# Kernel optimization log

Hardware: AMD Instinct MI355X
Metric: run time of the kernel (lower is better)

The kernel has to match this reference:

```python
import jax, jax.numpy as jnp
import numpy as np

B, M, H, K, D, L = 4, 1024, 1024, 16, 64, 1024
E, DH, TOPK = 8, 4096, 2
EPS = 1e-5


def _skew(X, pad_value):
    # X: [BK, M, L] -> [BK, M, M+L], row i shifted i steps right
    bk, m, l = X.shape
    X = jnp.pad(X, ((0, 0), (0, 0), (0, m + 1)), constant_values=pad_value)
    X = X.reshape(bk, -1)[:, :-m]
    return X.reshape(bk, m, m + l)


def _unskew(X):
    # X: [BK, M, M+L] -> [BK, M, L]
    bk, m, lp = X.shape
    l = lp - m
    X = X.reshape(bk, -1)
    X = jnp.pad(X, ((0, 0), (0, m)))
    X = X.reshape(bk, m, m + l + 1)
    return X[:, :, :l]


def layernorm(x, g, b):
    mu = jnp.mean(x, axis=-1, keepdims=True)
    var = jnp.var(x, axis=-1, keepdims=True)
    return (x - mu) * jax.lax.rsqrt(var + EPS) * g + b


def setup_inputs() -> dict:
    key = jax.random.key(0)
    ks = jax.random.split(key, 16)
    s = 1.0 / np.sqrt(H)
    inp = {
        'h': jax.random.normal(ks[0], (B, M, H), jnp.float32),
        'h_cache': jax.random.normal(ks[1], (B, L, H), jnp.float32),
        'key_pe': jax.random.normal(ks[2], (1, D, L), jnp.float32) * s,
        'wq': jax.random.normal(ks[3], (H, H), jnp.float32) * s,
        'wk': jax.random.normal(ks[4], (H, H), jnp.float32) * s,
        'wv': jax.random.normal(ks[5], (H, H), jnp.float32) * s,
        'wo': jax.random.normal(ks[6], (H, H), jnp.float32) * s,
        'norm1_g': jnp.ones((H,), jnp.float32),
        'norm1_b': jnp.zeros((H,), jnp.float32),
        'norm2_g': jnp.ones((H,), jnp.float32),
        'norm2_b': jnp.zeros((H,), jnp.float32),
        'moe_ln_g': jnp.ones((H,), jnp.float32),
        'moe_ln_b': jnp.zeros((H,), jnp.float32),
        'gate_w': jax.random.normal(ks[7], (H, E), jnp.float32) * s,
        'gate_b': jnp.zeros((E,), jnp.float32),
        'e_w1': jax.random.normal(ks[8], (E, H, DH), jnp.float32) * s,
        'e_b1': jnp.zeros((E, DH), jnp.float32),
        'e_w2': jax.random.normal(ks[9], (E, DH, H), jnp.float32) * (1.0 / np.sqrt(DH)),
        'e_b2': jnp.zeros((E, H), jnp.float32),
    }
    return inp


def _forward(h, h_cache, key_pe, wq, wk, wv, wo, norm1_g, norm1_b, norm2_g, norm2_b,
             moe_ln_g, moe_ln_b, gate_w, gate_b, e_w1, e_b1, e_w2, e_b2):
    h_all = jnp.concatenate([h_cache, h], axis=1)  # [B, L+M, H]

    def heads(x):  # [B, T, H] -> [B*K, T, D]
        b, t, _ = x.shape
        return x.reshape(b, t, K, D).transpose(0, 2, 1, 3).reshape(b * K, t, D)

    q = heads(h @ wq)          # [BK, M, D]
    k = heads(h_all @ wk)      # [BK, L+M, D]
    v = heads(h_all @ wv)      # [BK, L+M, D]

    attn_cont = jnp.einsum('bmd,bnd->bmn', q, k)      # [BK, M, L+M]
    attn_cont = _unskew(attn_cont)                     # [BK, M, L]
    attn_pos = jnp.einsum('bmd,dl->bml', q, key_pe[0])  # [BK, M, L]
    attn = (attn_cont + attn_pos) / np.sqrt(D)
    attn = jax.nn.softmax(attn, axis=-1)
    attn_sk = _skew(attn, 0.0)                         # [BK, M, M+L]
    out = jnp.einsum('bmn,bnd->bmd', attn_sk, v)       # [BK, M, D]
    out = out.reshape(B, K, M, D).transpose(0, 2, 1, 3).reshape(B, M, H)
    attn_out = out @ wo
    h = layernorm(h + attn_out, norm1_g, norm1_b)

    # --- MoE FFN (naive top-k gate, post-LN inside, dropout=0) ---
    x = h.reshape(-1, H)                               # [T, H]
    logits = x @ gate_w + gate_b                       # [T, E]
    vals, idx = jax.lax.top_k(logits, TOPK)            # [T, k]
    scores = jax.nn.softmax(vals, axis=-1)             # [T, k]
    hid = jax.nn.relu(jnp.einsum('th,ehd->etd', x, e_w1) + e_b1[:, None, :])
    all_out = jnp.einsum('etd,edh->eth', hid, e_w2) + e_b2[:, None, :]  # [E, T, H]
    sel = jnp.take_along_axis(all_out.transpose(1, 0, 2), idx[:, :, None], axis=1)  # [T, k, H]
    moe = jnp.sum(scores[:, :, None] * sel, axis=1)    # [T, H]
    core = layernorm(x + moe, moe_ln_g, moe_ln_b).reshape(B, M, H)
    h = layernorm(h + core, norm2_g, norm2_b)
    return h


def reference(h, h_cache, key_pe, wq, wk, wv, wo, norm1_g, norm1_b, norm2_g, norm2_b,
              moe_ln_g, moe_ln_b, gate_w, gate_b, e_w1, e_b1, e_w2, e_b2):
    return _forward(h, h_cache, key_pe, wq, wk, wv, wo, norm1_g, norm1_b, norm2_g,
                    norm2_b, moe_ln_g, moe_ln_b, gate_w, gate_b, e_w1, e_b1, e_w2, e_b2)
```

## Files before the change

### kernel.cpp

```cpp
#include <hip/hip_runtime.h>

typedef unsigned short u16;
typedef unsigned int u32;
typedef __attribute__((ext_vector_type(8))) __bf16 bf16x8;
typedef __attribute__((ext_vector_type(8))) _Float16 f16x8;
typedef __attribute__((ext_vector_type(4))) float f32x4;

__device__ __forceinline__ u16 f2bf(float f){
  unsigned int u = __float_as_uint(f);
  u += 0x7FFFu + ((u >> 16) & 1u);
  return (u16)(u >> 16);
}
__device__ __forceinline__ float bf2f(u16 s){
  return __uint_as_float(((unsigned int)s) << 16);
}
__device__ __forceinline__ void fsplit(float x, u16& hi, u16& lo){
  _Float16 h = (_Float16)x;
  float r = x - (float)h;
  _Float16 l = (_Float16)r;
  hi = *(u16*)&h; lo = *(u16*)&l;
}
__device__ __forceinline__ void gll16(const u16* g, u16* lds){
  __builtin_amdgcn_global_load_lds(
      (const __attribute__((address_space(1))) u32*)g,
      (__attribute__((address_space(3))) u32*)(u32)(unsigned long long)lds,
      16, 0, 0);
}


__global__ void zero8(int* c){ if (threadIdx.x < 8) c[threadIdx.x] = 0; }

__global__ __launch_bounds__(256)
void transpose_cvt_z(const float* __restrict__ in, u16* __restrict__ outp,
                     int R, int C, long zin, long zout)
{
  __shared__ float tile[32][33];
  in  += (long)blockIdx.z * zin;
  outp+= (long)blockIdx.z * zout;
  const int c0 = blockIdx.x << 5, r0 = blockIdx.y << 5;
  const int tx = threadIdx.x, ty = threadIdx.y;
  #pragma unroll
  for (int i = ty; i < 32; i += 8)
    tile[i][tx] = in[(long)(r0 + i) * C + c0 + tx];
  __syncthreads();
  #pragma unroll
  for (int i = ty; i < 32; i += 8)
    outp[(long)(c0 + i) * R + r0 + tx] = f2bf(tile[tx][i]);
}

__global__ __launch_bounds__(256)
void transpose_split4(const float* __restrict__ s0, const float* __restrict__ s1,
                      const float* __restrict__ s2, const float* __restrict__ s3,
                      u16* __restrict__ wall_h, u16* __restrict__ wall_l,
                      u16* __restrict__ wo_h, u16* __restrict__ wo_l)
{
  __shared__ float tile[32][33];
  const int z = blockIdx.z;
  const float* in = (z==0)?s0:(z==1)?s1:(z==2)?s2:s3;
  u16* oh = (z<3) ? (wall_h + (long)z*1024*1024) : wo_h;
  u16* ol = (z<3) ? (wall_l + (long)z*1024*1024) : wo_l;
  const int c0 = blockIdx.x << 5, r0 = blockIdx.y << 5;
  const int tx = threadIdx.x, ty = threadIdx.y;
  #pragma unroll
  for (int i = ty; i < 32; i += 8)
    tile[i][tx] = in[(long)(r0 + i) * 1024 + c0 + tx];
  __syncthreads();
  #pragma unroll
  for (int i = ty; i < 32; i += 8){
    u16 hh, ll;
    fsplit(tile[tx][i], hh, ll);
    oh[(long)(c0 + i) * 1024 + r0 + tx] = hh;
    ol[(long)(c0 + i) * 1024 + r0 + tx] = ll;
  }
}

__global__ __launch_bounds__(256)
void cvt_split_hall(const float* __restrict__ hc, const float* __restrict__ h,
                    u16* __restrict__ hi, u16* __restrict__ lo)
{
  long i4 = (long)blockIdx.x * 256 + threadIdx.x;
  long row = i4 >> 8;
  int c4 = (int)(i4 & 255);
  int b = (int)(row >> 11), tt = (int)(row & 2047);
  const float4* src = (const float4*)((tt < 1024) ? (hc + ((long)b*1024 + tt)*1024)
                                                  : (h  + ((long)b*1024 + (tt-1024))*1024));
  float4 v = src[c4];
  ushort4 h4, l4;
  fsplit(v.x, h4.x, l4.x); fsplit(v.y, h4.y, l4.y);
  fsplit(v.z, h4.z, l4.z); fsplit(v.w, h4.w, l4.w);
  ((ushort4*)hi)[i4] = h4;
  ((ushort4*)lo)[i4] = l4;
}

__global__ __launch_bounds__(128)
void pack_pe(const float* __restrict__ pe, u16* __restrict__ PEh, u16* __restrict__ PEl)
{
  const int jt = blockIdx.x;
  const int t = threadIdx.x;
  const int ks = t >> 6, lane = t & 63;
  const int fq = lane >> 4, fr = lane & 15;
  const long o = ((long)(jt*2 + ks)*64 + lane)*8;
  #pragma unroll
  for (int e = 0; e < 8; ++e){
    float v = pe[(long)(ks*32 + fq*8 + e)*1024 + jt*16 + fr];
    u16 hh, ll; fsplit(v, hh, ll);
    PEh[o+e] = hh; PEl[o+e] = ll;
  }
}


template<int EPI>
__global__ __launch_bounds__(256)
void gemm_sp(const u16* __restrict__ Ah_, const u16* __restrict__ Al_,
             const u16* __restrict__ Bh_, const u16* __restrict__ Bl_,
             float* __restrict__ C,
             u16* __restrict__ Kh, u16* __restrict__ Kl,
             u16* __restrict__ Vh, u16* __restrict__ Vl,
             u16* __restrict__ Qh, u16* __restrict__ Ql,
             int N, int Kd)
{
  __shared__ __align__(16) u16 Ahs[4096];
  __shared__ __align__(16) u16 Als[4096];
  __shared__ __align__(16) u16 Bhs[4096];
  __shared__ __align__(16) u16 Bls[4096];
  const int tm = blockIdx.y, tn = blockIdx.x;
  const int t = threadIdx.x;
  const int lane = t & 63, wv = t >> 6;
  const int wm = wv >> 1, wn = wv & 1;
  const int fr = lane & 15, fq = lane >> 4;

  const int r0l = 32*wv + (lane >> 2);
  const int r1l = r0l + 16;
  const int colu = (lane & 3) << 3;
  const long ar0 = (long)(tm*128 + r0l), ar1 = (long)(tm*128 + r1l);
  const long br0 = (long)(tn*128 + r0l), br1 = (long)(tn*128 + r1l);
  const u16* pah0 = Ah_ + ar0*Kd + colu;  const u16* pah1 = Ah_ + ar1*Kd + colu;
  const u16* pal0 = Al_ + ar0*Kd + colu;  const u16* pal1 = Al_ + ar1*Kd + colu;
  const u16* pbh0 = Bh_ + br0*Kd + colu;  const u16* pbh1 = Bh_ + br1*Kd + colu;
  const u16* pbl0 = Bl_ + br0*Kd + colu;  const u16* pbl1 = Bl_ + br1*Kd + colu;
  u16* lAh0 = Ahs + 1024*wv;  u16* lAh1 = lAh0 + 512;
  u16* lAl0 = Als + 1024*wv;  u16* lAl1 = lAl0 + 512;
  u16* lBh0 = Bhs + 1024*wv;  u16* lBh1 = lBh0 + 512;
  u16* lBl0 = Bls + 1024*wv;  u16* lBl1 = lBl0 + 512;

  f32x4 acc[4][4];
  const f32x4 z4 = {0.f,0.f,0.f,0.f};
  #pragma unroll
  for (int m=0;m<4;m++)
    #pragma unroll
    for (int n=0;n<4;n++) acc[m][n] = z4;

  const int nk = Kd >> 5;
  for (int kt = 0; kt < nk; ++kt) {
    const int ko = kt << 5;
    __syncthreads();
    gll16(pah0 + ko, lAh0); gll16(pah1 + ko, lAh1);
    gll16(pal0 + ko, lAl0); gll16(pal1 + ko, lAl1);
    gll16(pbh0 + ko, lBh0); gll16(pbh1 + ko, lBh1);
    gll16(pbl0 + ko, lBl0); gll16(pbl1 + ko, lBl1);
    __syncthreads();
    f16x8 afh[4], afl[4], bfh[4], bfl[4];
    #pragma unroll
    for (int m=0;m<4;m++){
      afh[m] = *(const f16x8*)(Ahs + (wm*64 + m*16 + fr)*32 + fq*8);
      afl[m] = *(const f16x8*)(Als + (wm*64 + m*16 + fr)*32 + fq*8);
    }
    #pragma unroll
    for (int n=0;n<4;n++){
      bfh[n] = *(const f16x8*)(Bhs + (wn*64 + n*16 + fr)*32 + fq*8);
      bfl[n] = *(const f16x8*)(Bls + (wn*64 + n*16 + fr)*32 + fq*8);
    }
    #pragma unroll
    for (int m=0;m<4;m++)
      #pragma unroll
      for (int n=0;n<4;n++){
        acc[m][n] = __builtin_amdgcn_mfma_f32_16x16x32_f16(afl[m], bfh[n], acc[m][n], 0, 0, 0);
        acc[m][n] = __builtin_amdgcn_mfma_f32_16x16x32_f16(afh[m], bfl[n], acc[m][n], 0, 0, 0);
        acc[m][n] = __builtin_amdgcn_mfma_f32_16x16x32_f16(afh[m], bfh[n], acc[m][n], 0, 0, 0);
      }
  }

  #pragma unroll
  for (int m=0;m<4;m++){
    #pragma unroll
    for (int j=0;j<4;j++){
      const long crow = (long)(tm*128 + wm*64 + m*16 + fq*4 + j);
      #pragma unroll
      for (int n=0;n<4;n++){
        const int c = tn*128 + wn*64 + n*16 + fr;
        float vv = acc[m][n][j];
        if (EPI == 0){
          C[crow * N + c] = vv;
        } else {
          const int b2 = (int)(crow >> 11), key = (int)(crow & 2047);
          u16 hh, ll; fsplit(vv, hh, ll);
          if (c < 1024){
            const int hd2 = c >> 6, dd = c & 63;
            const long addr = ((long)(b2*16 + hd2))*131072
                            + ((long)((key>>4)*2 + (dd>>5)))*512
                            + (((dd>>3)&3)*16 + (key&15))*8 + (dd&7);
            Kh[addr] = hh; Kl[addr] = ll;
          } else if (c < 2048){
            const int c2 = c - 1024;
            const int hd2 = c2 >> 6, dd = c2 & 63;
            const long addr = ((long)(b2*16 + hd2))*131072
                            + ((((long)(key>>4)*4 + (dd>>4))*2 + ((key>>3)&1)))*128
                            + (dd&15)*8 + (key&7);
            Vh[addr] = hh; Vl[addr] = ll;
          } else if (key >= 1024){
            const int c2 = c - 2048;
            const long qrow = (long)b2*1024 + (key - 1024);
            Qh[qrow*1024 + c2] = hh;
            Ql[qrow*1024 + c2] = ll;
          }
        }
      }
    }
  }
}


#define SJP 1032

__global__ __launch_bounds__(256)
void attn_mfma(const u16* __restrict__ qh, const u16* __restrict__ ql,
               const u16* __restrict__ Kph, const u16* __restrict__ Kpl,
               const u16* __restrict__ Vph, const u16* __restrict__ Vpl,
               const u16* __restrict__ PEh, const u16* __restrict__ PEl,
               u16* __restrict__ oh, u16* __restrict__ ol)
{
  __shared__ __align__(16) char smem[68608];
  float* Sj = (float*)smem;
  u16*   Ph = (u16*)smem;
  u16*   Pl = (u16*)(smem + 34048);
  const int bx = blockIdx.x;
  const int q0 = bx << 4;
  const int hd = blockIdx.y, b = blockIdx.z;
  const int t = threadIdx.x, lane = t & 63, wid = t >> 6;
  const int fr = lane & 15, fq = lane >> 4;
  const long plane = ((long)(b*16 + hd)) * 131072;

  f16x8 qfh[2], qfl[2];
  {
    const long qoff = ((long)(b*1024 + q0 + fr))*1024 + hd*64 + fq*8;
    qfh[0] = *(const f16x8*)(qh + qoff);
    qfh[1] = *(const f16x8*)(qh + qoff + 32);
    qfl[0] = *(const f16x8*)(ql + qoff);
    qfl[1] = *(const f16x8*)(ql + qoff + 32);
  }

  for (int base = 0; base < 65; base += 8){
    const int ta = base + wid;
    const int tb = base + wid + 4;
    const int tac = (ta < 65) ? ta : 64;
    const int tbc = (tb < 65) ? tb : 64;
    const u16* fA = Kph + plane + ((long)(bx + tac))*1024 + lane*8;
    const u16* fAl= Kpl + plane + ((long)(bx + tac))*1024 + lane*8;
    const u16* fB = Kph + plane + ((long)(bx + tbc))*1024 + lane*8;
    const u16* fBl= Kpl + plane + ((long)(bx + tbc))*1024 + lane*8;
    f32x4 accA = {0.f,0.f,0.f,0.f}, accB = {0.f,0.f,0.f,0.f};
    #pragma unroll
    for (int ks = 0; ks < 2; ++ks){
      f16x8 bhA = *(const f16x8*)(fA  + ks*512);
      f16x8 blA = *(const f16x8*)(fAl + ks*512);
      f16x8 bhB = *(const f16x8*)(fB  + ks*512);
      f16x8 blB = *(const f16x8*)(fBl + ks*512);
      accA = __builtin_amdgcn_mfma_f32_16x16x32_f16(qfl[ks], bhA, accA, 0, 0, 0);
      accB = __builtin_amdgcn_mfma_f32_16x16x32_f16(qfl[ks], bhB, accB, 0, 0, 0);
      accA = __builtin_amdgcn_mfma_f32_16x16x32_f16(qfh[ks], blA, accA, 0, 0, 0);
      accB = __builtin_amdgcn_mfma_f32_16x16x32_f16(qfh[ks], blB, accB, 0, 0, 0);
      accA = __builtin_amdgcn_mfma_f32_16x16x32_f16(qfh[ks], bhA, accA, 0, 0, 0);
      accB = __builtin_amdgcn_mfma_f32_16x16x32_f16(qfh[ks], bhB, accB, 0, 0, 0);
    }
    if (ta < 65){
      const int ca = tac*16 + fr;
      #pragma unroll
      for (int jj = 0; jj < 4; ++jj){
        const int row = fq*4 + jj;
        const int j = ca - row;
        if (j >= 0 && j < 1024) Sj[row*SJP + j] = accA[jj];
      }
    }
    if (tb < 65){
      const int cb = tbc*16 + fr;
      #pragma unroll
      for (int jj = 0; jj < 4; ++jj){
        const int row = fq*4 + jj;
        const int j = cb - row;
        if (j >= 0 && j < 1024) Sj[row*SJP + j] = accB[jj];
      }
    }
  }
  __syncthreads();

  for (int base = 0; base < 64; base += 8){
    const int ta = base + wid, tb = base + wid + 4;
    const u16* fA = PEh + ((long)ta)*1024 + lane*8;
    const u16* fAl= PEl + ((long)ta)*1024 + lane*8;
    const u16* fB = PEh + ((long)tb)*1024 + lane*8;
    const u16* fBl= PEl + ((long)tb)*1024 + lane*8;
    f32x4 accA = {0.f,0.f,0.f,0.f}, accB = {0.f,0.f,0.f,0.f};
    #pragma unroll
    for (int ks = 0; ks < 2; ++ks){
      f16x8 bhA = *(const f16x8*)(fA  + ks*512);
      f16x8 blA = *(const f16x8*)(fAl + ks*512);
      f16x8 bhB = *(const f16x8*)(fB  + ks*512);
      f16x8 blB = *(const f16x8*)(fBl + ks*512);
      accA = __builtin_amdgcn_mfma_f32_16x16x32_f16(qfl[ks], bhA, accA, 0, 0, 0);
      accB = __builtin_amdgcn_mfma_f32_16x16x32_f16(qfl[ks], bhB, accB, 0, 0, 0);
      accA = __builtin_amdgcn_mfma_f32_16x16x32_f16(qfh[ks], blA, accA, 0, 0, 0);
      accB = __builtin_amdgcn_mfma_f32_16x16x32_f16(qfh[ks], blB, accB, 0, 0, 0);
      accA = __builtin_amdgcn_mfma_f32_16x16x32_f16(qfh[ks], bhA, accA, 0, 0, 0);
      accB = __builtin_amdgcn_mfma_f32_16x16x32_f16(qfh[ks], bhB, accB, 0, 0, 0);
    }
    const int ja = ta*16 + fr, jb = tb*16 + fr;
    #pragma unroll
    for (int jj = 0; jj < 4; ++jj){
      const int row = fq*4 + jj;
      Sj[row*SJP + ja] += accA[jj];
      Sj[row*SJP + jb] += accB[jj];
    }
  }
  __syncthreads();

  {
    const int r = t >> 4, g = t & 15;
    float sv[64];
    float mx = -3.0e38f;
    #pragma unroll
    for (int m = 0; m < 64; ++m){
      float x = Sj[r*SJP + g + (m<<4)] * 0.125f;
      sv[m] = x; mx = fmaxf(mx, x);
    }
    #pragma unroll
    for (int o = 8; o; o >>= 1) mx = fmaxf(mx, __shfl_xor(mx, o, 64));
    float sum = 0.f;
    #pragma unroll
    for (int m = 0; m < 64; ++m){ sv[m] = __expf(sv[m] - mx); sum += sv[m]; }
    #pragma unroll
    for (int o = 8; o; o >>= 1) sum += __shfl_xor(sum, o, 64);
    const float inv = 1.f / sum;
    __syncthreads();
    for (int i = t; i < 17024; i += 256) ((unsigned*)smem)[i] = 0;
    __syncthreads();
    #pragma unroll
    for (int m = 0; m < 64; ++m){
      float p = sv[m] * inv;
      u16 hh, ll; fsplit(p, hh, ll);
      const int c = r + g + (m<<4);
      Ph[r*1064 + c] = hh;
      Pl[r*1064 + c] = ll;
    }
  }
  __syncthreads();

  {
    f32x4 acc0 = {0.f,0.f,0.f,0.f}, acc1 = {0.f,0.f,0.f,0.f};
    const int qq = fq & 1;
    for (int ks = 0; ks < 33; ++ks){
      int kc16 = bx + 2*ks + (fq >> 1);
      if (kc16 > 127) kc16 = 127;
      const long vo = plane + (((long)kc16*4 + wid)*2 + qq)*128 + fr*8;
      f16x8 vh = *(const f16x8*)(Vph + vo);
      f16x8 vl = *(const f16x8*)(Vpl + vo);
      f16x8 ah = *(const f16x8*)(Ph + fr*1064 + ks*32 + fq*8);
      f16x8 al = *(const f16x8*)(Pl + fr*1064 + ks*32 + fq*8);
      f32x4& a = (ks & 1) ? acc1 : acc0;
      a = __builtin_amdgcn_mfma_f32_16x16x32_f16(al, vh, a, 0, 0, 0);
      a = __builtin_amdgcn_mfma_f32_16x16x32_f16(ah, vl, a, 0, 0, 0);
      a = __builtin_amdgcn_mfma_f32_16x16x32_f16(ah, vh, a, 0, 0, 0);
    }
    #pragma unroll
    for (int jj = 0; jj < 4; ++jj){
      float v = acc0[jj] + acc1[jj];
      u16 hh, ll; fsplit(v, hh, ll);
      const int row = fq*4 + jj;
      const long o = ((long)(b*1024 + q0 + row))*1024 + hd*64 + wid*16 + fr;
      oh[o] = hh; ol[o] = ll;
    }
  }
}


template<bool GATHER, bool RELU>
__global__ __launch_bounds__(256)
void gemm_bt(const u16* __restrict__ A, const u16* __restrict__ Bt, u16* __restrict__ Cp,
             const float* __restrict__ bias, int N, int Kd, int maxA,
             const int* __restrict__ offs, const int* __restrict__ counts,
             const int* __restrict__ gather, int ebase)
{
  __shared__ __align__(16) u16 As[2][4096];
  __shared__ __align__(16) u16 Bs[2][4096];
  const int z = blockIdx.z;
  const int e = ebase + z;
  const int rbase = offs[e];
  const int cnt   = counts[e];
  const int tm = blockIdx.y, tn = blockIdx.x;
  if (tm * 128 >= cnt) return;
  const u16* BtE = Bt + (long)z * N * Kd;
  const float* biasE = bias + (long)e * N;

  const int t = threadIdx.x;
  const int lane = t & 63, wv = t >> 6;
  const int wm = wv >> 1, wn = wv & 1;
  const int fr = lane & 15, fq = lane >> 4;

  const int r0l = 32*wv + (lane >> 2);
  const int r1l = r0l + 16;
  const int colu = (lane & 3) << 3;
  auto amap = [&](int rl)->long{
    int r = tm*128 + rl;
    int rc = (r < cnt) ? r : (cnt - 1);
    if (GATHER){
      int gi = rbase + rc; gi = (gi < 0) ? 0 : ((gi > 8191) ? 8191 : gi);
      int tok = gather[gi];
      tok = (tok < 0) ? 0 : ((tok >= maxA) ? (maxA - 1) : tok);
      return (long)tok;
    }
    return (long)(rbase + rc);
  };
  const long ar0 = amap(r0l), ar1 = amap(r1l);
  const long br0 = (long)(tn*128 + r0l), br1 = (long)(tn*128 + r1l);
  const u16* pa0 = A + ar0*Kd + colu;    const u16* pa1 = A + ar1*Kd + colu;
  const u16* pb0 = BtE + br0*Kd + colu;  const u16* pb1 = BtE + br1*Kd + colu;

  f32x4 acc[4][4];
  const f32x4 z4 = {0.f,0.f,0.f,0.f};
  #pragma unroll
  for (int m=0;m<4;m++)
    #pragma unroll
    for (int n=0;n<4;n++) acc[m][n] = z4;

  auto issue = [&](int bufi, int kt){
    const int ko = kt << 5;
    gll16(pa0 + ko, As[bufi] + 1024*wv);
    gll16(pa1 + ko, As[bufi] + 1024*wv + 512);
    gll16(pb0 + ko, Bs[bufi] + 1024*wv);
    gll16(pb1 + ko, Bs[bufi] + 1024*wv + 512);
  };

  const int nk = Kd >> 5;
  issue(0, 0);
  for (int kt = 0; kt < nk; ++kt) {
    const int cur = kt & 1;
    __syncthreads();
    if (kt + 1 < nk) issue(cur ^ 1, kt + 1);
    bf16x8 af[4], bfv[4];
    #pragma unroll
    for (int m=0;m<4;m++) af[m]  = *(const bf16x8*)(As[cur] + (wm*64 + m*16 + fr)*32 + fq*8);
    #pragma unroll
    for (int n=0;n<4;n++) bfv[n] = *(const bf16x8*)(Bs[cur] + (wn*64 + n*16 + fr)*32 + fq*8);
    #pragma unroll
    for (int m=0;m<4;m++)
      #pragma unroll
      for (int n=0;n<4;n++)
        acc[m][n] = __builtin_amdgcn_mfma_f32_16x16x32_bf16(af[m], bfv[n], acc[m][n], 0, 0, 0);
  }

  #pragma unroll
  for (int m=0;m<4;m++){
    #pragma unroll
    for (int j=0;j<4;j++){
      const int r = tm*128 + wm*64 + m*16 + fq*4 + j;
      if (r >= cnt) continue;
      const long crow = (long)(rbase + r);
      #pragma unroll
      for (int n=0;n<4;n++){
        const int c = tn*128 + wn*64 + n*16 + fr;
        float vv = acc[m][n][j] + biasE[c];
        if (RELU) vv = fmaxf(vv, 0.f);
        Cp[crow * N + c] = f2bf(vv);
      }
    }
  }
}


__device__ __forceinline__ void block_reduce2(float& s1, float& s2){
  #pragma unroll
  for (int o = 32; o; o >>= 1){
    s1 += __shfl_xor(s1, o, 64);
    s2 += __shfl_xor(s2, o, 64);
  }
  __shared__ float r1[4], r2[4];
  const int wid = threadIdx.x >> 6;
  if ((threadIdx.x & 63) == 0){ r1[wid] = s1; r2[wid] = s2; }
  __syncthreads();
  s1 = r1[0] + r1[1] + r1[2] + r1[3];
  s2 = r2[0] + r2[1] + r2[2] + r2[3];
  __syncthreads();
}

__global__ __launch_bounds__(256)
void add_ln_kernel(const float* __restrict__ a, const float* __restrict__ r,
                   const float* __restrict__ g, const float* __restrict__ bb,
                   float* __restrict__ of, u16* __restrict__ ob)
{
  const long row = blockIdx.x;
  const int t = threadIdx.x;
  float y[4]; float sum = 0.f, sq = 0.f;
  #pragma unroll
  for (int i = 0; i < 4; ++i){
    const long idx = row*1024 + t + (i<<8);
    float vv = a[idx] + r[idx];
    y[i] = vv; sum += vv; sq += vv*vv;
  }
  block_reduce2(sum, sq);
  const float mu = sum * (1.f/1024.f);
  const float var = fmaxf(sq * (1.f/1024.f) - mu*mu, 0.f);
  const float rs = rsqrtf(var + 1e-5f);
  #pragma unroll
  for (int i = 0; i < 4; ++i){
    const int hcol = t + (i<<8);
    float o = (y[i] - mu) * rs * g[hcol] + bb[hcol];
    of[row*1024 + hcol] = o;
    ob[row*1024 + hcol] = f2bf(o);
  }
}

__global__ __launch_bounds__(256)
void gate_kernel(const float* __restrict__ x, const float* __restrict__ gw,
                 const float* __restrict__ gb, int* __restrict__ eidx,
                 float* __restrict__ esc, int* __restrict__ counts)
{
  const long row = blockIdx.x;
  const int t = threadIdx.x;
  float a[8];
  #pragma unroll
  for (int e=0;e<8;e++) a[e]=0.f;
  for (int hcol = t; hcol < 1024; hcol += 256){
    float xv = x[row*1024 + hcol];
    const float* gr = gw + hcol*8;
    #pragma unroll
    for (int e=0;e<8;e++) a[e] += xv * gr[e];
  }
  #pragma unroll
  for (int e=0;e<8;e++)
    #pragma unroll
    for (int o=32;o;o>>=1) a[e] += __shfl_xor(a[e], o, 64);
  __shared__ float red[4][8];
  const int wid = t >> 6;
  if ((t & 63)==0){
    #pragma unroll
    for (int e=0;e<8;e++) red[wid][e]=a[e];
  }
  __syncthreads();
  if (t == 0){
    float l[8];
    #pragma unroll
    for (int e=0;e<8;e++) l[e] = red[0][e]+red[1][e]+red[2][e]+red[3][e] + gb[e];
    int i0 = 0; float v0 = l[0];
    #pragma unroll
    for (int e=1;e<8;e++) if (l[e] > v0){ v0=l[e]; i0=e; }
    int i1 = -1; float v1 = -3.0e38f;
    #pragma unroll
    for (int e=0;e<8;e++) if (e != i0 && l[e] > v1){ v1=l[e]; i1=e; }
    float e1 = __expf(v1 - v0);
    float den = 1.f + e1;
    eidx[row*2+0]=i0; eidx[row*2+1]=i1;
    esc[row*2+0]=1.f/den; esc[row*2+1]=e1/den;
    atomicAdd(&counts[i0],1); atomicAdd(&counts[i1],1);
  }
}

__global__ void scan_kernel(const int* __restrict__ counts, int* __restrict__ offs,
                            int* __restrict__ curs)
{
  if (threadIdx.x == 0 && blockIdx.x == 0){
    int acc = 0;
    for (int e=0;e<8;e++){ offs[e]=acc; curs[e]=acc; acc += counts[e]; }
  }
}

__global__ __launch_bounds__(256)
void scatter_kernel(const int* __restrict__ eidx, int* __restrict__ curs,
                    int* __restrict__ stok, int* __restrict__ ppos)
{
  int id = blockIdx.x*256 + threadIdx.x;
  if (id >= 8192) return;
  int e = eidx[id];
  e = (e < 0) ? 0 : ((e > 7) ? 7 : e);
  int pos = atomicAdd(&curs[e], 1);
  pos = (pos < 0) ? 0 : ((pos > 8191) ? 8191 : pos);
  stok[pos] = id >> 1;
  ppos[id] = pos;
}

__global__ __launch_bounds__(256)
void moe_combine_ln(const float* __restrict__ h1, const u16* __restrict__ pout,
                    const float* __restrict__ esc, const int* __restrict__ ppos,
                    const float* __restrict__ mg, const float* __restrict__ mb,
                    const float* __restrict__ n2g, const float* __restrict__ n2b,
                    float* __restrict__ outp)
{
  const long row = blockIdx.x;
  const int t = threadIdx.x;
  int p0i = ppos[row*2+0], p1i = ppos[row*2+1];
  p0i = (p0i < 0) ? 0 : ((p0i > 8191) ? 8191 : p0i);
  p1i = (p1i < 0) ? 0 : ((p1i > 8191) ? 8191 : p1i);
  const long p0 = p0i, p1 = p1i;
  const float s0 = esc[row*2+0], s1 = esc[row*2+1];
  float x[4], y[4];
  float sum=0.f, sq=0.f;
  #pragma unroll
  for (int i=0;i<4;i++){
    const int hcol = t + (i<<8);
    const long idx = row*1024 + hcol;
    float xv = h1[idx];
    float m = s0 * bf2f(pout[p0*1024 + hcol]) + s1 * bf2f(pout[p1*1024 + hcol]);
    x[i]=xv; y[i]=xv+m; sum+=y[i]; sq+=y[i]*y[i];
  }
  block_reduce2(sum, sq);
  float mu = sum*(1.f/1024.f), var = fmaxf(sq*(1.f/1024.f)-mu*mu, 0.f), rs = rsqrtf(var+1e-5f);
  float zz[4]; float sum2=0.f, sq2=0.f;
  #pragma unroll
  for (int i=0;i<4;i++){
    const int hcol = t + (i<<8);
    float core = (y[i]-mu)*rs*mg[hcol]+mb[hcol];
    zz[i] = x[i] + core; sum2+=zz[i]; sq2+=zz[i]*zz[i];
  }
  block_reduce2(sum2, sq2);
  float mu2 = sum2*(1.f/1024.f), var2 = fmaxf(sq2*(1.f/1024.f)-mu2*mu2, 0.f), rs2 = rsqrtf(var2+1e-5f);
  #pragma unroll
  for (int i=0;i<4;i++){
    const int hcol = t + (i<<8);
    outp[row*1024 + hcol] = (zz[i]-mu2)*rs2*n2g[hcol]+n2b[hcol];
  }
}


extern "C" void kernel_launch(void* const* d_in, const int* in_sizes, int n_in,
                              void* d_out, int out_size, void* d_ws, size_t ws_size,
                              hipStream_t stream)
{
  const float* h      = (const float*)d_in[0];
  const float* hc     = (const float*)d_in[1];
  const float* key_pe = (const float*)d_in[2];
  const float* wq     = (const float*)d_in[3];
  const float* wk     = (const float*)d_in[4];
  const float* wv     = (const float*)d_in[5];
  const float* wo     = (const float*)d_in[6];
  const float* n1g    = (const float*)d_in[7];
  const float* n1b    = (const float*)d_in[8];
  const float* n2g    = (const float*)d_in[9];
  const float* n2b    = (const float*)d_in[10];
  const float* mlg    = (const float*)d_in[11];
  const float* mlb    = (const float*)d_in[12];
  const float* gw     = (const float*)d_in[13];
  const float* gb     = (const float*)d_in[14];
  const float* ew1    = (const float*)d_in[15];
  const float* eb1    = (const float*)d_in[16];
  const float* ew2    = (const float*)d_in[17];
  const float* eb2    = (const float*)d_in[18];
  float* outp = (float*)d_out;

  const size_t MB = 1ull << 20;
  char* base = (char*)d_ws;
  int*   counts = (int*)(base);
  int*   offs   = (int*)(base + 256);
  int*   curs   = (int*)(base + 512);
  int*   eidx   = (int*)(base + 1024);
  float* esc    = (float*)(base + 64*1024);
  int*   stok   = (int*)(base + 128*1024);
  int*   ppos   = (int*)(base + 192*1024);
  u16*   PEp_h  = (u16*)(base + 1*MB);
  u16*   PEp_l  = (u16*)(base + 1*MB + 256*1024);
  u16*   hall_h = (u16*)(base + 2*MB);
  float* h1     = (float*)(base + 2*MB);
  u16*   hall_l = (u16*)(base + 18*MB);
  u16*   h1b    = (u16*)(base + 18*MB);
  u16*   wall_h = (u16*)(base + 34*MB);
  u16*   wall_l = (u16*)(base + 40*MB);
  u16*   woT_h  = (u16*)(base + 46*MB);
  u16*   woT_l  = (u16*)(base + 48*MB);
  u16*   wTg    = (u16*)(base + 34*MB);
  u16*   qh     = (u16*)(base + 50*MB);
  u16*   ql     = (u16*)(base + 58*MB);
  float* aproj  = (float*)(base + 50*MB);
  u16*   Kp_h   = (u16*)(base + 66*MB);
  u16*   Kp_l   = (u16*)(base + 82*MB);
  u16*   Vp_h   = (u16*)(base + 98*MB);
  u16*   Vp_l   = (u16*)(base + 114*MB);
  u16*   xhid   = (u16*)(base + 66*MB);
  u16*   aout_h = (u16*)(base + 130*MB);
  u16*   aout_l = (u16*)(base + 138*MB);
  u16*   pout   = (u16*)(base + 130*MB);

  zero8<<<1, 64, 0, stream>>>(counts);
  dim3 tb32(32, 8);

  cvt_split_hall<<<8192, 256, 0, stream>>>(hc, h, hall_h, hall_l);
  pack_pe<<<64, 128, 0, stream>>>(key_pe, PEp_h, PEp_l);
  transpose_split4<<<dim3(32,32,4), tb32, 0, stream>>>(wk, wv, wq, wo,
                                                       wall_h, wall_l, woT_h, woT_l);

  gemm_sp<4><<<dim3(24,64), 256, 0, stream>>>(hall_h, hall_l, wall_h, wall_l, nullptr,
                                              Kp_h, Kp_l, Vp_h, Vp_l, qh, ql, 3072, 1024);

  attn_mfma<<<dim3(64,16,4), 256, 0, stream>>>(qh, ql, Kp_h, Kp_l, Vp_h, Vp_l, PEp_h, PEp_l, aout_h, aout_l);

  gemm_sp<0><<<dim3(8,32), 256, 0, stream>>>(aout_h, aout_l, woT_h, woT_l, aproj,
                                             nullptr, nullptr, nullptr, nullptr, nullptr, nullptr, 1024, 1024);
  add_ln_kernel<<<4096, 256, 0, stream>>>(h, aproj, n1g, n1b, h1, h1b);

  gate_kernel<<<4096, 256, 0, stream>>>(h1, gw, gb, eidx, esc, counts);
  scan_kernel<<<1, 64, 0, stream>>>(counts, offs, curs);
  scatter_kernel<<<32, 256, 0, stream>>>(eidx, curs, stok, ppos);

  for (int g = 0; g < 2; ++g){
    transpose_cvt_z<<<dim3(128,32,4), tb32, 0, stream>>>(
        ew1 + (long)g*4*1024*4096, wTg, 1024, 4096, 4096L*1024, 4096L*1024);
    gemm_bt<true, true ><<<dim3(32,64,4), 256, 0, stream>>>(
        h1b, wTg, xhid, eb1, 4096, 1024, 4096, offs, counts, stok, g*4);
  }
  for (int g = 0; g < 2; ++g){
    transpose_cvt_z<<<dim3(32,128,4), tb32, 0, stream>>>(
        ew2 + (long)g*4*4096*1024, wTg, 4096, 1024, 4096L*1024, 4096L*1024);
    gemm_bt<false, false><<<dim3(8,64,4), 256, 0, stream>>>(
        xhid, wTg, pout, eb2, 1024, 4096, 8192, offs, counts, nullptr, g*4);
  }

  moe_combine_ln<<<4096, 256, 0, stream>>>(h1, pout, esc, ppos, mlg, mlb, n2g, n2b, outp);
}
```

Before: 1.073 ms.

## Double-buffer output-projection GEMM, prefetch attention fragments, swizzle blocks, fuse gate into LN

Adds a double-buffered LDS variant of the split-precision GEMM and uses it for the output projection, so the next K tile loads while the current one computes. The attention kernel now prefetches the next K, positional-embedding, V and P fragments into registers, remaps a 1D grid so adjacent blocks spread across heads and batches, and pads the P row stride to reduce LDS bank conflicts. The MoE gate logits and top-2 selection are folded into the add+layernorm kernel, which removes one launch and a re-read of h1. These raise register and LDS pressure, which may lower occupancy.

```diff
diff --git a/kernel.cpp b/kernel.cpp
--- a/kernel.cpp
+++ b/kernel.cpp
@@ -109,7 +109,7 @@
 }
 
 
-template<int EPI>
+template<int EPI, bool DBUF>
 __global__ __launch_bounds__(256)
 void gemm_sp(const u16* __restrict__ Ah_, const u16* __restrict__ Al_,
              const u16* __restrict__ Bh_, const u16* __restrict__ Bl_,
@@ -119,10 +119,10 @@
              u16* __restrict__ Qh, u16* __restrict__ Ql,
              int N, int Kd)
 {
-  __shared__ __align__(16) u16 Ahs[4096];
-  __shared__ __align__(16) u16 Als[4096];
-  __shared__ __align__(16) u16 Bhs[4096];
-  __shared__ __align__(16) u16 Bls[4096];
+  __shared__ __align__(16) u16 Ahs[(DBUF?2:1)*4096];
+  __shared__ __align__(16) u16 Als[(DBUF?2:1)*4096];
+  __shared__ __align__(16) u16 Bhs[(DBUF?2:1)*4096];
+  __shared__ __align__(16) u16 Bls[(DBUF?2:1)*4096];
   const int tm = blockIdx.y, tn = blockIdx.x;
   const int t = threadIdx.x;
   const int lane = t & 63, wv = t >> 6;
@@ -138,10 +138,6 @@
   const u16* pal0 = Al_ + ar0*Kd + colu;  const u16* pal1 = Al_ + ar1*Kd + colu;
   const u16* pbh0 = Bh_ + br0*Kd + colu;  const u16* pbh1 = Bh_ + br1*Kd + colu;
   const u16* pbl0 = Bl_ + br0*Kd + colu;  const u16* pbl1 = Bl_ + br1*Kd + colu;
-  u16* lAh0 = Ahs + 1024*wv;  u16* lAh1 = lAh0 + 512;
-  u16* lAl0 = Als + 1024*wv;  u16* lAl1 = lAl0 + 512;
-  u16* lBh0 = Bhs + 1024*wv;  u16* lBh1 = lBh0 + 512;
-  u16* lBl0 = Bls + 1024*wv;  u16* lBl1 = lBl0 + 512;
 
   f32x4 acc[4][4];
   const f32x4 z4 = {0.f,0.f,0.f,0.f};
@@ -150,25 +146,42 @@
     #pragma unroll
     for (int n=0;n<4;n++) acc[m][n] = z4;
 
+  auto issue = [&](int bufi, int kt){
+    const int ko = kt << 5;
+    u16* a0 = Ahs + bufi*4096 + 1024*wv;
+    u16* l0 = Als + bufi*4096 + 1024*wv;
+    u16* b0 = Bhs + bufi*4096 + 1024*wv;
+    u16* c0 = Bls + bufi*4096 + 1024*wv;
+    gll16(pah0 + ko, a0); gll16(pah1 + ko, a0 + 512);
+    gll16(pal0 + ko, l0); gll16(pal1 + ko, l0 + 512);
+    gll16(pbh0 + ko, b0); gll16(pbh1 + ko, b0 + 512);
+    gll16(pbl0 + ko, c0); gll16(pbl1 + ko, c0 + 512);
+  };
+
   const int nk = Kd >> 5;
+  if (DBUF) issue(0, 0);
   for (int kt = 0; kt < nk; ++kt) {
-    const int ko = kt << 5;
-    __syncthreads();
-    gll16(pah0 + ko, lAh0); gll16(pah1 + ko, lAh1);
-    gll16(pal0 + ko, lAl0); gll16(pal1 + ko, lAl1);
-    gll16(pbh0 + ko, lBh0); gll16(pbh1 + ko, lBh1);
-    gll16(pbl0 + ko, lBl0); gll16(pbl1 + ko, lBl1);
-    __syncthreads();
+    int cur;
+    if (DBUF){
+      cur = kt & 1;
+      __syncthreads();
+      if (kt + 1 < nk) issue(cur ^ 1, kt + 1);
+    } else {
+      cur = 0;
+      __syncthreads();
+      issue(0, kt);
+      __syncthreads();
+    }
     f16x8 afh[4], afl[4], bfh[4], bfl[4];
     #pragma unroll
     for (int m=0;m<4;m++){
-      afh[m] = *(const f16x8*)(Ahs + (wm*64 + m*16 + fr)*32 + fq*8);
-      afl[m] = *(const f16x8*)(Als + (wm*64 + m*16 + fr)*32 + fq*8);
+      afh[m] = *(const f16x8*)(Ahs + cur*4096 + (wm*64 + m*16 + fr)*32 + fq*8);
+      afl[m] = *(const f16x8*)(Als + cur*4096 + (wm*64 + m*16 + fr)*32 + fq*8);
     }
     #pragma unroll
     for (int n=0;n<4;n++){
-      bfh[n] = *(const f16x8*)(Bhs + (wn*64 + n*16 + fr)*32 + fq*8);
-      bfl[n] = *(const f16x8*)(Bls + (wn*64 + n*16 + fr)*32 + fq*8);
+      bfh[n] = *(const f16x8*)(Bhs + cur*4096 + (wn*64 + n*16 + fr)*32 + fq*8);
+      bfl[n] = *(const f16x8*)(Bls + cur*4096 + (wn*64 + n*16 + fr)*32 + fq*8);
     }
     #pragma unroll
     for (int m=0;m<4;m++)
@@ -221,6 +234,7 @@
 
 
 #define SJP 1032
+#define PJP 1066
 
 __global__ __launch_bounds__(256)
 void attn_mfma(const u16* __restrict__ qh, const u16* __restrict__ ql,
@@ -232,10 +246,13 @@
   __shared__ __align__(16) char smem[68608];
   float* Sj = (float*)smem;
   u16*   Ph = (u16*)smem;
-  u16*   Pl = (u16*)(smem + 34048);
-  const int bx = blockIdx.x;
+  u16*   Pl = (u16*)(smem + 34112);
+  const int id = blockIdx.x;
+  const int sw = (id & 7) * 512 + (id >> 3);
+  const int bx = sw & 63;
+  const int hd = (sw >> 6) & 15;
+  const int b  = sw >> 10;
   const int q0 = bx << 4;
-  const int hd = blockIdx.y, b = blockIdx.z;
   const int t = threadIdx.x, lane = t & 63, wid = t >> 6;
   const int fr = lane & 15, fq = lane >> 4;
   const long plane = ((long)(b*16 + hd)) * 131072;
@@ -249,76 +266,94 @@
     qfl[1] = *(const f16x8*)(ql + qoff + 32);
   }
 
-  for (int base = 0; base < 65; base += 8){
-    const int ta = base + wid;
-    const int tb = base + wid + 4;
-    const int tac = (ta < 65) ? ta : 64;
-    const int tbc = (tb < 65) ? tb : 64;
-    const u16* fA = Kph + plane + ((long)(bx + tac))*1024 + lane*8;
-    const u16* fAl= Kpl + plane + ((long)(bx + tac))*1024 + lane*8;
-    const u16* fB = Kph + plane + ((long)(bx + tbc))*1024 + lane*8;
-    const u16* fBl= Kpl + plane + ((long)(bx + tbc))*1024 + lane*8;
-    f32x4 accA = {0.f,0.f,0.f,0.f}, accB = {0.f,0.f,0.f,0.f};
-    #pragma unroll
-    for (int ks = 0; ks < 2; ++ks){
-      f16x8 bhA = *(const f16x8*)(fA  + ks*512);
-      f16x8 blA = *(const f16x8*)(fAl + ks*512);
-      f16x8 bhB = *(const f16x8*)(fB  + ks*512);
-      f16x8 blB = *(const f16x8*)(fBl + ks*512);
-      accA = __builtin_amdgcn_mfma_f32_16x16x32_f16(qfl[ks], bhA, accA, 0, 0, 0);
-      accB = __builtin_amdgcn_mfma_f32_16x16x32_f16(qfl[ks], bhB, accB, 0, 0, 0);
-      accA = __builtin_amdgcn_mfma_f32_16x16x32_f16(qfh[ks], blA, accA, 0, 0, 0);
-      accB = __builtin_amdgcn_mfma_f32_16x16x32_f16(qfh[ks], blB, accB, 0, 0, 0);
-      accA = __builtin_amdgcn_mfma_f32_16x16x32_f16(qfh[ks], bhA, accA, 0, 0, 0);
-      accB = __builtin_amdgcn_mfma_f32_16x16x32_f16(qfh[ks], bhB, accB, 0, 0, 0);
-    }
-    if (ta < 65){
-      const int ca = tac*16 + fr;
+  {
+    f16x8 cA[4], cB[4], nA[4], nB[4];
+    auto kfrag = [&](int tile, f16x8* d){
+      const int tc = (tile < 65) ? tile : 64;
+      const u16* f  = Kph + plane + ((long)(bx + tc))*1024 + lane*8;
+      const u16* fl = Kpl + plane + ((long)(bx + tc))*1024 + lane*8;
+      d[0] = *(const f16x8*)(f);
+      d[1] = *(const f16x8*)(fl);
+      d[2] = *(const f16x8*)(f + 512);
+      d[3] = *(const f16x8*)(fl + 512);
+    };
+    kfrag(wid, cA); kfrag(wid + 4, cB);
+    for (int base = 0; base < 65; base += 8){
+      const int ta = base + wid, tb = base + wid + 4;
+      if (base + 8 < 65){ kfrag(base + 8 + wid, nA); kfrag(base + 12 + wid, nB); }
+      f32x4 accA = {0.f,0.f,0.f,0.f}, accB = {0.f,0.f,0.f,0.f};
+      accA = __builtin_amdgcn_mfma_f32_16x16x32_f16(qfl[0], cA[0], accA, 0, 0, 0);
+      accB = __builtin_amdgcn_mfma_f32_16x16x32_f16(qfl[0], cB[0], accB, 0, 0, 0);
+      accA = __builtin_amdgcn_mfma_f32_16x16x32_f16(qfh[0], cA[1], accA, 0, 0, 0);
+      accB = __builtin_amdgcn_mfma_f32_16x16x32_f16(qfh[0], cB[1], accB, 0, 0, 0);
+      accA = __builtin_amdgcn_mfma_f32_16x16x32_f16(qfh[0], cA[0], accA, 0, 0, 0);
+      accB = __builtin_amdgcn_mfma_f32_16x16x32_f16(qfh[0], cB[0], accB, 0, 0, 0);
+      accA = __builtin_amdgcn_mfma_f32_16x16x32_f16(qfl[1], cA[2], accA, 0, 0, 0);
+      accB = __builtin_amdgcn_mfma_f32_16x16x32_f16(qfl[1], cB[2], accB, 0, 0, 0);
+      accA = __builtin_amdgcn_mfma_f32_16x16x32_f16(qfh[1], cA[3], accA, 0, 0, 0);
+      accB = __builtin_amdgcn_mfma_f32_16x16x32_f16(qfh[1], cB[3], accB, 0, 0, 0);
+      accA = __builtin_amdgcn_mfma_f32_16x16x32_f16(qfh[1], cA[2], accA, 0, 0, 0);
+      accB = __builtin_amdgcn_mfma_f32_16x16x32_f16(qfh[1], cB[2], accB, 0, 0, 0);
+      if (ta < 65){
+        const int ca = ta*16 + fr;
+        #pragma unroll
+        for (int jj = 0; jj < 4; ++jj){
+          const int row = fq*4 + jj;
+          const int j = ca - row;
+          if (j >= 0 && j < 1024) Sj[row*SJP + j] = accA[jj];
+        }
+      }
+      if (tb < 65){
+        const int cb = tb*16 + fr;
+        #pragma unroll
+        for (int jj = 0; jj < 4; ++jj){
+          const int row = fq*4 + jj;
+          const int j = cb - row;
+          if (j >= 0 && j < 1024) Sj[row*SJP + j] = accB[jj];
+        }
+      }
+      #pragma unroll
+      for (int i = 0; i < 4; ++i){ cA[i] = nA[i]; cB[i] = nB[i]; }
+    }
+  }
+  __syncthreads();
+
+  {
+    f16x8 cA[4], cB[4], nA[4], nB[4];
+    auto pefrag = [&](int tile, f16x8* d){
+      const u16* f  = PEh + ((long)tile)*1024 + lane*8;
+      const u16* fl = PEl + ((long)tile)*1024 + lane*8;
+      d[0] = *(const f16x8*)(f);
+      d[1] = *(const f16x8*)(fl);
+      d[2] = *(const f16x8*)(f + 512);
+      d[3] = *(const f16x8*)(fl + 512);
+    };
+    pefrag(wid, cA); pefrag(wid + 4, cB);
+    for (int base = 0; base < 64; base += 8){
+      const int ta = base + wid, tb = base + wid + 4;
+      if (base + 8 < 64){ pefrag(base + 8 + wid, nA); pefrag(base + 12 + wid, nB); }
+      f32x4 accA = {0.f,0.f,0.f,0.f}, accB = {0.f,0.f,0.f,0.f};
+      accA = __builtin_amdgcn_mfma_f32_16x16x32_f16(qfl[0], cA[0], accA, 0, 0, 0);
+      accB = __builtin_amdgcn_mfma_f32_16x16x32_f16(qfl[0], cB[0], accB, 0, 0, 0);
+      accA = __builtin_amdgcn_mfma_f32_16x16x32_f16(qfh[0], cA[1], accA, 0, 0, 0);
+      accB = __builtin_amdgcn_mfma_f32_16x16x32_f16(qfh[0], cB[1], accB, 0, 0, 0);
+      accA = __builtin_amdgcn_mfma_f32_16x16x32_f16(qfh[0], cA[0], accA, 0, 0, 0);
+      accB = __builtin_amdgcn_mfma_f32_16x16x32_f16(qfh[0], cB[0], accB, 0, 0, 0);
+      accA = __builtin_amdgcn_mfma_f32_16x16x32_f16(qfl[1], cA[2], accA, 0, 0, 0);
+      accB = __builtin_amdgcn_mfma_f32_16x16x32_f16(qfl[1], cB[2], accB, 0, 0, 0);
+      accA = __builtin_amdgcn_mfma_f32_16x16x32_f16(qfh[1], cA[3], accA, 0, 0, 0);
+      accB = __builtin_amdgcn_mfma_f32_16x16x32_f16(qfh[1], cB[3], accB, 0, 0, 0);
+      accA = __builtin_amdgcn_mfma_f32_16x16x32_f16(qfh[1], cA[2], accA, 0, 0, 0);
+      accB = __builtin_amdgcn_mfma_f32_16x16x32_f16(qfh[1], cB[2], accB, 0, 0, 0);
+      const int ja = ta*16 + fr, jb = tb*16 + fr;
       #pragma unroll
       for (int jj = 0; jj < 4; ++jj){
         const int row = fq*4 + jj;
-        const int j = ca - row;
-        if (j >= 0 && j < 1024) Sj[row*SJP + j] = accA[jj];
+        Sj[row*SJP + ja] += accA[jj];
+        Sj[row*SJP + jb] += accB[jj];
       }
-    }
-    if (tb < 65){
-      const int cb = tbc*16 + fr;
       #pragma unroll
-      for (int jj = 0; jj < 4; ++jj){
-        const int row = fq*4 + jj;
-        const int j = cb - row;
-        if (j >= 0 && j < 1024) Sj[row*SJP + j] = accB[jj];
-      }
-    }
-  }
-  __syncthreads();
-
-  for (int base = 0; base < 64; base += 8){
-    const int ta = base + wid, tb = base + wid + 4;
-    const u16* fA = PEh + ((long)ta)*1024 + lane*8;
-    const u16* fAl= PEl + ((long)ta)*1024 + lane*8;
-    const u16* fB = PEh + ((long)tb)*1024 + lane*8;
-    const u16* fBl= PEl + ((long)tb)*1024 + lane*8;
-    f32x4 accA = {0.f,0.f,0.f,0.f}, accB = {0.f,0.f,0.f,0.f};
-    #pragma unroll
-    for (int ks = 0; ks < 2; ++ks){
-      f16x8 bhA = *(const f16x8*)(fA  + ks*512);
-      f16x8 blA = *(const f16x8*)(fAl + ks*512);
-      f16x8 bhB = *(const f16x8*)(fB  + ks*512);
-      f16x8 blB = *(const f16x8*)(fBl + ks*512);
-      accA = __builtin_amdgcn_mfma_f32_16x16x32_f16(qfl[ks], bhA, accA, 0, 0, 0);
-      accB = __builtin_amdgcn_mfma_f32_16x16x32_f16(qfl[ks], bhB, accB, 0, 0, 0);
-      accA = __builtin_amdgcn_mfma_f32_16x16x32_f16(qfh[ks], blA, accA, 0, 0, 0);
-      accB = __builtin_amdgcn_mfma_f32_16x16x32_f16(qfh[ks], blB, accB, 0, 0, 0);
-      accA = __builtin_amdgcn_mfma_f32_16x16x32_f16(qfh[ks], bhA, accA, 0, 0, 0);
-      accB = __builtin_amdgcn_mfma_f32_16x16x32_f16(qfh[ks], bhB, accB, 0, 0, 0);
-    }
-    const int ja = ta*16 + fr, jb = tb*16 + fr;
-    #pragma unroll
-    for (int jj = 0; jj < 4; ++jj){
-      const int row = fq*4 + jj;
-      Sj[row*SJP + ja] += accA[jj];
-      Sj[row*SJP + jb] += accB[jj];
+      for (int i = 0; i < 4; ++i){ cA[i] = nA[i]; cB[i] = nB[i]; }
     }
   }
   __syncthreads();
@@ -341,15 +376,15 @@
     for (int o = 8; o; o >>= 1) sum += __shfl_xor(sum, o, 64);
     const float inv = 1.f / sum;
     __syncthreads();
-    for (int i = t; i < 17024; i += 256) ((unsigned*)smem)[i] = 0;
+    for (int i = t; i < 17056; i += 256) ((unsigned*)smem)[i] = 0;
     __syncthreads();
     #pragma unroll
     for (int m = 0; m < 64; ++m){
       float p = sv[m] * inv;
       u16 hh, ll; fsplit(p, hh, ll);
       const int c = r + g + (m<<4);
-      Ph[r*1064 + c] = hh;
-      Pl[r*1064 + c] = ll;
+      Ph[r*PJP + c] = hh;
+      Pl[r*PJP + c] = ll;
     }
   }
   __syncthreads();
@@ -357,18 +392,26 @@
   {
     f32x4 acc0 = {0.f,0.f,0.f,0.f}, acc1 = {0.f,0.f,0.f,0.f};
     const int qq = fq & 1;
-    for (int ks = 0; ks < 33; ++ks){
+    auto vfrag = [&](int ks, f16x8& vh, f16x8& vl){
       int kc16 = bx + 2*ks + (fq >> 1);
       if (kc16 > 127) kc16 = 127;
       const long vo = plane + (((long)kc16*4 + wid)*2 + qq)*128 + fr*8;
-      f16x8 vh = *(const f16x8*)(Vph + vo);
-      f16x8 vl = *(const f16x8*)(Vpl + vo);
-      f16x8 ah = *(const f16x8*)(Ph + fr*1064 + ks*32 + fq*8);
-      f16x8 al = *(const f16x8*)(Pl + fr*1064 + ks*32 + fq*8);
+      vh = *(const f16x8*)(Vph + vo);
+      vl = *(const f16x8*)(Vpl + vo);
+    };
+    auto pfrag = [&](int ks, f16x8& ah, f16x8& al){
+      ah = *(const f16x8*)(Ph + fr*PJP + ks*32 + fq*8);
+      al = *(const f16x8*)(Pl + fr*PJP + ks*32 + fq*8);
+    };
+    f16x8 cvh, cvl, cah, cal, nvh, nvl, nah, nal;
+    vfrag(0, cvh, cvl); pfrag(0, cah, cal);
+    for (int ks = 0; ks < 33; ++ks){
+      if (ks + 1 < 33){ vfrag(ks + 1, nvh, nvl); pfrag(ks + 1, nah, nal); }
       f32x4& a = (ks & 1) ? acc1 : acc0;
-      a = __builtin_amdgcn_mfma_f32_16x16x32_f16(al, vh, a, 0, 0, 0);
-      a = __builtin_amdgcn_mfma_f32_16x16x32_f16(ah, vl, a, 0, 0, 0);
-      a = __builtin_amdgcn_mfma_f32_16x16x32_f16(ah, vh, a, 0, 0, 0);
+      a = __builtin_amdgcn_mfma_f32_16x16x32_f16(cal, cvh, a, 0, 0, 0);
+      a = __builtin_amdgcn_mfma_f32_16x16x32_f16(cah, cvl, a, 0, 0, 0);
+      a = __builtin_amdgcn_mfma_f32_16x16x32_f16(cah, cvh, a, 0, 0, 0);
+      cvh = nvh; cvl = nvl; cah = nah; cal = nal;
     }
     #pragma unroll
     for (int jj = 0; jj < 4; ++jj){
@@ -492,9 +535,11 @@
 }
 
 __global__ __launch_bounds__(256)
-void add_ln_kernel(const float* __restrict__ a, const float* __restrict__ r,
-                   const float* __restrict__ g, const float* __restrict__ bb,
-                   float* __restrict__ of, u16* __restrict__ ob)
+void add_ln_gate(const float* __restrict__ a, const float* __restrict__ r,
+                 const float* __restrict__ g, const float* __restrict__ bb,
+                 const float* __restrict__ gw, const float* __restrict__ gb,
+                 float* __restrict__ of, u16* __restrict__ ob,
+                 int* __restrict__ eidx, float* __restrict__ esc, int* __restrict__ counts)
 {
   const long row = blockIdx.x;
   const int t = threadIdx.x;
@@ -509,40 +554,28 @@
   const float mu = sum * (1.f/1024.f);
   const float var = fmaxf(sq * (1.f/1024.f) - mu*mu, 0.f);
   const float rs = rsqrtf(var + 1e-5f);
+  float ge[8];
+  #pragma unroll
+  for (int e=0;e<8;e++) ge[e]=0.f;
   #pragma unroll
   for (int i = 0; i < 4; ++i){
     const int hcol = t + (i<<8);
     float o = (y[i] - mu) * rs * g[hcol] + bb[hcol];
     of[row*1024 + hcol] = o;
     ob[row*1024 + hcol] = f2bf(o);
-  }
-}
-
-__global__ __launch_bounds__(256)
-void gate_kernel(const float* __restrict__ x, const float* __restrict__ gw,
-                 const float* __restrict__ gb, int* __restrict__ eidx,
-                 float* __restrict__ esc, int* __restrict__ counts)
-{
-  const long row = blockIdx.x;
-  const int t = threadIdx.x;
-  float a[8];
-  #pragma unroll
-  for (int e=0;e<8;e++) a[e]=0.f;
-  for (int hcol = t; hcol < 1024; hcol += 256){
-    float xv = x[row*1024 + hcol];
     const float* gr = gw + hcol*8;
     #pragma unroll
-    for (int e=0;e<8;e++) a[e] += xv * gr[e];
+    for (int e=0;e<8;e++) ge[e] += o * gr[e];
   }
   #pragma unroll
   for (int e=0;e<8;e++)
     #pragma unroll
-    for (int o=32;o;o>>=1) a[e] += __shfl_xor(a[e], o, 64);
+    for (int o=32;o;o>>=1) ge[e] += __shfl_xor(ge[e], o, 64);
   __shared__ float red[4][8];
   const int wid = t >> 6;
   if ((t & 63)==0){
     #pragma unroll
-    for (int e=0;e<8;e++) red[wid][e]=a[e];
+    for (int e=0;e<8;e++) red[wid][e]=ge[e];
   }
   __syncthreads();
   if (t == 0){
@@ -694,16 +727,15 @@
   transpose_split4<<<dim3(32,32,4), tb32, 0, stream>>>(wk, wv, wq, wo,
                                                        wall_h, wall_l, woT_h, woT_l);
 
-  gemm_sp<4><<<dim3(24,64), 256, 0, stream>>>(hall_h, hall_l, wall_h, wall_l, nullptr,
-                                              Kp_h, Kp_l, Vp_h, Vp_l, qh, ql, 3072, 1024);
-
-  attn_mfma<<<dim3(64,16,4), 256, 0, stream>>>(qh, ql, Kp_h, Kp_l, Vp_h, Vp_l, PEp_h, PEp_l, aout_h, aout_l);
-
-  gemm_sp<0><<<dim3(8,32), 256, 0, stream>>>(aout_h, aout_l, woT_h, woT_l, aproj,
-                                             nullptr, nullptr, nullptr, nullptr, nullptr, nullptr, 1024, 1024);
-  add_ln_kernel<<<4096, 256, 0, stream>>>(h, aproj, n1g, n1b, h1, h1b);
-
-  gate_kernel<<<4096, 256, 0, stream>>>(h1, gw, gb, eidx, esc, counts);
+  gemm_sp<4,false><<<dim3(24,64), 256, 0, stream>>>(hall_h, hall_l, wall_h, wall_l, nullptr,
+                                                    Kp_h, Kp_l, Vp_h, Vp_l, qh, ql, 3072, 1024);
+
+  attn_mfma<<<4096, 256, 0, stream>>>(qh, ql, Kp_h, Kp_l, Vp_h, Vp_l, PEp_h, PEp_l, aout_h, aout_l);
+
+  gemm_sp<0,true><<<dim3(8,32), 256, 0, stream>>>(aout_h, aout_l, woT_h, woT_l, aproj,
+                                                  nullptr, nullptr, nullptr, nullptr, nullptr, nullptr, 1024, 1024);
+  add_ln_gate<<<4096, 256, 0, stream>>>(h, aproj, n1g, n1b, gw, gb, h1, h1b, eidx, esc, counts);
+
   scan_kernel<<<1, 64, 0, stream>>>(counts, offs, curs);
   scatter_kernel<<<32, 256, 0, stream>>>(eidx, curs, stok, ppos);
 
```

Result: no change. 1.059 ms (-1.3%).
